# Kernel tuning notes

Hardware: AMD Instinct MI355X
Metric: run time of the kernel (lower is better)

## Reference

```python
import jax, jax.numpy as jnp
import numpy as np

B, L, N, HID, NH, HD, SH, SW, MH = 1, 512, 2048, 2048, 16, 128, 64, 32, 8192


def _rms(x, w, eps=1e-6):
    return x * jax.lax.rsqrt(jnp.mean(x * x, axis=-1, keepdims=True) + eps) * w


def _adaln(x, emb, W, b, nw):
    e = jax.nn.silu(emb) @ W + b  # [B, 6*hid]
    sh_m, sc_m, g_m, sh_p, sc_p, g_p = jnp.split(e, 6, axis=-1)
    xm = _rms(x, nw) * (1.0 + sc_m[:, None]) + sh_m[:, None]
    return xm, g_m, sh_p, sc_p, g_p


def _rope(x, rope):
    # x: [B, H, S, D], rope: [S, 1, D]
    f = rope[:, 0]  # [S, D]
    cos = jnp.repeat(f[:, 0::2], 2, axis=-1)[None, None]
    sin = jnp.repeat(f[:, 1::2], 2, axis=-1)[None, None]
    xr = x.reshape(*x.shape[:-1], -1, 2)
    x_rot = jnp.stack([-xr[..., 1], xr[..., 0]], axis=-1).reshape(x.shape)
    return x * cos + x_rot * sin


def _sdpa(q, k, v, scale):
    s = jnp.einsum('bhqd,bhkd->bhqk', q, k) * scale
    return jnp.einsum('bhqk,bhkd->bhqd', jax.nn.softmax(s, axis=-1), v)


def _mlp(x, w1, b1, w2, b2):
    return jax.nn.gelu(x @ w1 + b1, approximate=True) @ w2 + b2


def setup_inputs() -> dict:
    key = jax.random.key(0)
    ks = iter(jax.random.split(key, 32))
    r = lambda *s: jax.random.normal(next(ks), s, dtype=jnp.float32) * 0.02
    inp = {
        'txt': jax.random.normal(next(ks), (B, L, HID), dtype=jnp.float32),
        'img': jax.random.normal(next(ks), (B, N, HID), dtype=jnp.float32),
        'vec': jax.random.normal(next(ks), (B, HID), dtype=jnp.float32),
        'rope': jax.random.normal(next(ks), (N, 1, HD), dtype=jnp.float32),
        'sol_temperature': jax.random.uniform(next(ks), (B, 64), dtype=jnp.float32),
        'sol_spatial': jax.random.normal(next(ks), (B, 8, 8), dtype=jnp.float32),
        'ada_img_w': r(HID, 6 * HID), 'ada_img_b': jnp.zeros(6 * HID, jnp.float32), 'ada_img_nw': jnp.ones(HID, jnp.float32),
        'ada_txt_w': r(HID, 6 * HID), 'ada_txt_b': jnp.zeros(6 * HID, jnp.float32), 'ada_txt_nw': jnp.ones(HID, jnp.float32),
        'txt_qkv_w': r(HID, 3 * HID), 'img_qkv_w': r(HID, 3 * HID),
        'txt_out_w': r(HID, HID), 'img_out_w': r(HID, HID),
        'mod_w': r(NH) * 5.0, 'mod_b': r(NH) * 5.0,
        'img_n2_w': jnp.ones(HID, jnp.float32), 'txt_n2_w': jnp.ones(HID, jnp.float32),
        'img_fc1_w': r(HID, MH), 'img_fc1_b': jnp.zeros(MH, jnp.float32),
        'img_fc2_w': r(MH, HID), 'img_fc2_b': jnp.zeros(HID, jnp.float32),
        'txt_fc1_w': r(HID, MH), 'txt_fc1_b': jnp.zeros(MH, jnp.float32),
        'txt_fc2_w': r(MH, HID), 'txt_fc2_b': jnp.zeros(HID, jnp.float32),
        'spatial_h': SH, 'spatial_w': SW,
    }
    return inp


def reference(txt, img, vec, rope, sol_temperature, sol_spatial,
              ada_img_w, ada_img_b, ada_img_nw, ada_txt_w, ada_txt_b, ada_txt_nw,
              txt_qkv_w, img_qkv_w, txt_out_w, img_out_w, mod_w, mod_b,
              img_n2_w, txt_n2_w, img_fc1_w, img_fc1_b, img_fc2_w, img_fc2_b,
              txt_fc1_w, txt_fc1_b, txt_fc2_w, txt_fc2_b, spatial_h, spatial_w):
    b, l, hid = txt.shape
    n = img.shape[1]
    nh = mod_w.shape[0]
    hd = hid // nh
    scale = hd ** (-0.5)

    img_n, img_g, img_shp, img_scp, img_gp = _adaln(img, vec, ada_img_w, ada_img_b, ada_img_nw)
    txt_n, txt_g, txt_shp, txt_scp, txt_gp = _adaln(txt, vec, ada_txt_w, ada_txt_b, ada_txt_nw)

    def qkv(x, w, s):
        p = (x @ w).reshape(b, s, 3, nh, hd).transpose(2, 0, 3, 1, 4)  # [3,B,H,S,D]
        return p[0], p[1], p[2]

    tq, tk, tv = qkv(txt_n, txt_qkv_w, l)
    iq, ik, iv = qkv(img_n, img_qkv_w, n)
    iq = _rope(iq, rope)
    ik = _rope(ik, rope)

    # SOL spatial modulation: bilinear upsample (align_corners=False) + 1x1 conv + exp(clamp)
    sol_up = jax.image.resize(sol_spatial, (b, spatial_h, spatial_w), 'bilinear')
    mod = sol_up[:, None] * mod_w[None, :, None, None] + mod_b[None, :, None, None]
    mod = jnp.exp(jnp.clip(mod, -2.0, 2.0)).reshape(b, nh, n, 1)
    iq = iq * mod
    ik = ik * mod

    k = jnp.concatenate([tk, ik], axis=2)  # [B,H,L+N,D]
    v = jnp.concatenate([tv, iv], axis=2)

    txt_attn = _sdpa(tq, k, v, scale).transpose(0, 2, 1, 3).reshape(b, l, hid) @ txt_out_w

    temp = jnp.clip(jnp.mean(sol_temperature, axis=1, keepdims=True), 0.1)  # [B,1]
    s_eff = jnp.sqrt(scale / temp)[:, :, None, None]  # [B,1,1,1]
    img_attn = _sdpa(iq * s_eff, k * s_eff, v, 1.0).transpose(0, 2, 1, 3).reshape(b, n, hid) @ img_out_w

    txt = txt + txt_g[:, None] * txt_attn
    img = img + img_g[:, None] * img_attn

    txt_in = _rms(txt, txt_n2_w) * (1.0 + txt_scp[:, None]) + txt_shp[:, None]
    img_in = _rms(img, img_n2_w) * (1.0 + img_scp[:, None]) + img_shp[:, None]
    txt = txt + txt_gp[:, None] * _mlp(txt_in, txt_fc1_w, txt_fc1_b, txt_fc2_w, txt_fc2_b)
    img = img + img_gp[:, None] * _mlp(img_in, img_fc1_w, img_fc1_b, img_fc2_w, img_fc2_b)
    return txt, img
```

## Files before the change

kernel.cpp:

```cpp
#include <hip/hip_runtime.h>

typedef short short8 __attribute__((ext_vector_type(8)));
typedef float f32x4 __attribute__((ext_vector_type(4)));

__device__ __forceinline__ unsigned short f2bu(float f) {
  unsigned u = __builtin_bit_cast(unsigned, f);
  u += 0x7fffu + ((u >> 16) & 1u);
  return (unsigned short)(u >> 16);
}

__device__ __forceinline__ unsigned short f2bt(float f) {
  return (unsigned short)(__builtin_bit_cast(unsigned, f) >> 16);
}

__device__ __forceinline__ float b2f(unsigned short b) {
  unsigned u = (unsigned)b << 16;
  return __builtin_bit_cast(float, u);
}

__device__ __forceinline__ float gelu_t(float x) {
  float x3 = x * x * x;
  float t = tanhf(0.7978845608028654f * (x + 0.044715f * x3));
  return 0.5f * x * (1.f + t);
}

__device__ __forceinline__ void gload16(const void* g, void* l) {
  __builtin_amdgcn_global_load_lds(
      (const __attribute__((address_space(1))) void*)g,
      (__attribute__((address_space(3))) void*)l, 16, 0, 0);
}

__global__ __launch_bounds__(256) void prep_small(
    const float* __restrict__ vec, const float* __restrict__ sol_t,
    float* __restrict__ silu_vec, float* __restrict__ scales) {
  __shared__ float red[4];
  int t = threadIdx.x;
  float v = (t < 64) ? sol_t[t] : 0.f;
#pragma unroll
  for (int o = 32; o > 0; o >>= 1) v += __shfl_down(v, o);
  if ((t & 63) == 0) red[t >> 6] = v;
  __syncthreads();
  if (t == 0) {
    float m = (red[0] + red[1] + red[2] + red[3]) * (1.f / 64.f);
    m = fmaxf(m, 0.1f);
    const float sc = 0.08838834764831845f;
    const float l2e = 1.4426950408889634f;
    scales[0] = sc * l2e;
    scales[1] = sc / m * l2e;
  }
  for (int k = t; k < 2048; k += 256) {
    float x = vec[k];
    silu_vec[k] = x / (1.f + expf(-x));
  }
}

__global__ __launch_bounds__(256) void mod_kernel(
    const float* __restrict__ S, const float* __restrict__ mw,
    const float* __restrict__ mb, float* __restrict__ modb) {
  int idx = blockIdx.x * 256 + threadIdx.x;
  int h = idx >> 11, n = idx & 2047;
  int y = n >> 5, x = n & 31;
  float cy = (y + 0.5f) * 0.125f - 0.5f;
  float cx = (x + 0.5f) * 0.25f - 0.5f;
  int y0 = (int)floorf(cy); float fy = cy - (float)y0;
  int x0 = (int)floorf(cx); float fx = cx - (float)x0;
  int y0c = min(max(y0, 0), 7), y1c = min(max(y0 + 1, 0), 7);
  int x0c = min(max(x0, 0), 7), x1c = min(max(x0 + 1, 0), 7);
  float v = (1.f - fy) * ((1.f - fx) * S[y0c * 8 + x0c] + fx * S[y0c * 8 + x1c]) +
            fy * ((1.f - fx) * S[y1c * 8 + x0c] + fx * S[y1c * 8 + x1c]);
  float t = v * mw[h] + mb[h];
  t = fminf(fmaxf(t, -2.f), 2.f);
  modb[idx] = expf(t);
}

__global__ __launch_bounds__(256) void ada_gemv(
    const float* __restrict__ sv,
    const float* __restrict__ Wi, const float* __restrict__ bi,
    const float* __restrict__ Wt, const float* __restrict__ bt,
    float* __restrict__ ei, float* __restrict__ et) {
  __shared__ float red[4][64];
  const float* W = blockIdx.y ? Wt : Wi;
  const float* bb = blockIdx.y ? bt : bi;
  float* e = blockIdx.y ? et : ei;
  int jl = threadIdx.x & 63, ks = threadIdx.x >> 6;
  int j = blockIdx.x * 64 + jl;
  float acc = 0.f;
  int k0 = ks * 512;
#pragma unroll 4
  for (int k = 0; k < 512; ++k) acc += sv[k0 + k] * W[(size_t)(k0 + k) * 12288 + j];
  red[ks][jl] = acc;
  __syncthreads();
  if (ks == 0) e[j] = red[0][jl] + red[1][jl] + red[2][jl] + red[3][jl] + bb[j];
}

__global__ __launch_bounds__(256) void norm1_kernel(
    const float* __restrict__ txt, const float* __restrict__ img,
    const float* __restrict__ nw_t, const float* __restrict__ nw_i,
    const float* __restrict__ e_t, const float* __restrict__ e_i,
    unsigned short* __restrict__ out) {
  __shared__ float red[4];
  int r = blockIdx.x, t = threadIdx.x;
  bool ist = r < 512;
  const float* X = ist ? txt + (size_t)r * 2048 : img + (size_t)(r - 512) * 2048;
  const float* nw = ist ? nw_t : nw_i;
  const float* e = ist ? e_t : e_i;
  const float4* xr = reinterpret_cast<const float4*>(X);
  float4 v0 = xr[t * 2], v1 = xr[t * 2 + 1];
  float ss = v0.x * v0.x + v0.y * v0.y + v0.z * v0.z + v0.w * v0.w +
             v1.x * v1.x + v1.y * v1.y + v1.z * v1.z + v1.w * v1.w;
#pragma unroll
  for (int o = 32; o > 0; o >>= 1) ss += __shfl_down(ss, o);
  if ((t & 63) == 0) red[t >> 6] = ss;
  __syncthreads();
  float rinv = rsqrtf((red[0] + red[1] + red[2] + red[3]) * (1.f / 2048.f) + 1e-6f);
  int c0 = t * 8;
  float xv[8] = {v0.x, v0.y, v0.z, v0.w, v1.x, v1.y, v1.z, v1.w};
  short8 ov;
#pragma unroll
  for (int i = 0; i < 8; ++i) {
    int c = c0 + i;
    float y = xv[i] * rinv * nw[c] * (1.f + e[2048 + c]) + e[c];
    ov[i] = (short)f2bu(y);
  }
  *reinterpret_cast<short8*>(out + (size_t)r * 2048 + c0) = ov;
}

__global__ __launch_bounds__(256) void res1_rms(
    const float* __restrict__ txt, const float* __restrict__ img,
    const float* __restrict__ P0,
    const float* __restrict__ e_t, const float* __restrict__ e_i,
    const float* __restrict__ nw_t, const float* __restrict__ nw_i,
    float* __restrict__ out, unsigned short* __restrict__ actA) {
  __shared__ float red[4];
  int r = blockIdx.x, t = threadIdx.x;
  bool ist = r < 512;
  const float* X = ist ? txt + (size_t)r * 2048 : img + (size_t)(r - 512) * 2048;
  const float* e = ist ? e_t : e_i;
  const float* nw = ist ? nw_t : nw_i;
  int c0 = t * 8;
  const float* p0 = P0 + (size_t)r * 2048 + c0;
  float o[8];
  float ss = 0.f;
#pragma unroll
  for (int i = 0; i < 8; i += 4) {
    float4 x = *reinterpret_cast<const float4*>(X + c0 + i);
    float4 a = *reinterpret_cast<const float4*>(p0 + i);
    float4 g = *reinterpret_cast<const float4*>(e + 4096 + c0 + i);
    o[i + 0] = x.x + g.x * a.x;
    o[i + 1] = x.y + g.y * a.y;
    o[i + 2] = x.z + g.z * a.z;
    o[i + 3] = x.w + g.w * a.w;
    ss += o[i] * o[i] + o[i + 1] * o[i + 1] + o[i + 2] * o[i + 2] + o[i + 3] * o[i + 3];
  }
  *reinterpret_cast<float4*>(out + (size_t)r * 2048 + c0) =
      make_float4(o[0], o[1], o[2], o[3]);
  *reinterpret_cast<float4*>(out + (size_t)r * 2048 + c0 + 4) =
      make_float4(o[4], o[5], o[6], o[7]);
#pragma unroll
  for (int of = 32; of > 0; of >>= 1) ss += __shfl_down(ss, of);
  if ((t & 63) == 0) red[t >> 6] = ss;
  __syncthreads();
  float rinv = rsqrtf((red[0] + red[1] + red[2] + red[3]) * (1.f / 2048.f) + 1e-6f);
  short8 ov;
#pragma unroll
  for (int i = 0; i < 8; ++i) {
    int c = c0 + i;
    float y = o[i] * rinv * nw[c] * (1.f + e[8192 + c]) + e[6144 + c];
    ov[i] = (short)f2bu(y);
  }
  *reinterpret_cast<short8*>(actA + (size_t)r * 2048 + c0) = ov;
}

__global__ __launch_bounds__(256) void transpose_w2(
    const float* __restrict__ W0, const float* __restrict__ W1,
    unsigned short* __restrict__ B0, unsigned short* __restrict__ B1,
    int K, int N) {
  __shared__ float tile[64][65];
  const float* W = blockIdx.z ? W1 : W0;
  unsigned short* Bt = blockIdx.z ? B1 : B0;
  int n0 = blockIdx.x * 64, k0 = blockIdx.y * 64;
  int t = threadIdx.x;
  int rn = (t & 15) * 4, rk = t >> 4;
#pragma unroll
  for (int j = 0; j < 4; ++j) {
    float4 v = *reinterpret_cast<const float4*>(
        W + (size_t)(k0 + rk + j * 16) * N + n0 + rn);
    tile[rk + j * 16][rn + 0] = v.x;
    tile[rk + j * 16][rn + 1] = v.y;
    tile[rk + j * 16][rn + 2] = v.z;
    tile[rk + j * 16][rn + 3] = v.w;
  }
  __syncthreads();
  int wn = t >> 2, wk = (t & 3) * 16;
  unsigned pk[8];
#pragma unroll
  for (int i = 0; i < 8; ++i) {
    float lo = tile[wk + 2 * i][wn], hi = tile[wk + 2 * i + 1][wn];
    pk[i] = (unsigned)f2bu(lo) | ((unsigned)f2bu(hi) << 16);
  }
  unsigned short* dst = Bt + (size_t)(n0 + wn) * K + k0 + wk;
  *reinterpret_cast<int4*>(dst) = make_int4(pk[0], pk[1], pk[2], pk[3]);
  *reinterpret_cast<int4*>(dst + 8) = make_int4(pk[4], pk[5], pk[6], pk[7]);
}

__global__ __launch_bounds__(256) void transpose_v(
    const unsigned short* __restrict__ V, unsigned short* __restrict__ Vt) {
  __shared__ unsigned short tile[32][33];
  int h = blockIdx.z;
  int s0 = blockIdx.x * 32, d0 = blockIdx.y * 32;
  int tx = threadIdx.x, ty = threadIdx.y;
  const unsigned short* src = V + (size_t)h * 2560 * 128;
  unsigned short* dst = Vt + (size_t)h * 128 * 2560;
#pragma unroll
  for (int j = 0; j < 32; j += 8)
    tile[ty + j][tx] = src[(size_t)(s0 + ty + j) * 128 + d0 + tx];
  __syncthreads();
#pragma unroll
  for (int j = 0; j < 32; j += 8)
    dst[(size_t)(d0 + ty + j) * 2560 + s0 + tx] = tile[tx][ty + j];
}

struct GemmP {
  const unsigned short *A, *Bt_t, *Bt_i;
  float* C;
  unsigned short* Cb;
  const float *bias_t, *bias_i;
  const float *rope, *modb;
  unsigned short *q_txt, *q_img, *k_cat, *v_cat;
  const float* scales;
  const float *ga_t, *ga_i;
  int Mb_t;
  int N, K, KS;
};

template <int EPI>
__global__ __launch_bounds__(256) void gemm2(GemmP p) {
  __shared__ __align__(16) char GRAW[65536];
  int4* sAb = reinterpret_cast<int4*>(GRAW);
  int4* sBb = reinterpret_cast<int4*>(GRAW + 32768);
  const int NB = gridDim.x, MBT = gridDim.y;
  int nwg = NB * MBT;
  int orig = blockIdx.y * NB + blockIdx.x;
  int qq = nwg >> 3, rr = nwg & 7, xcd = orig & 7, base = orig >> 3;
  int sw = (xcd < rr ? xcd * (qq + 1) : rr * (qq + 1) + (xcd - rr) * qq) + base;
  int bx = sw / MBT, by = sw % MBT;
  const bool is_t = by < p.Mb_t;
  const unsigned short* Bt = is_t ? p.Bt_t : p.Bt_i;
  const int m0 = by * 128, n0 = bx * 128;
  const int z = blockIdx.z;
  const int Kz = p.K / p.KS, kbeg = z * Kz, kend = kbeg + Kz;
  const int tid = threadIdx.x;
  const int w = tid >> 6, l = tid & 63, lr = l & 15, lg = l >> 4;
  const int wm = (w >> 1) * 64, wn = (w & 1) * 64;
  f32x4 acc[4][4] = {};
  const int4* Ag = reinterpret_cast<const int4*>(p.A);
  const int4* Bg = reinterpret_cast<const int4*>(Bt);
  const int K8 = p.K >> 3;
  int srow[4], sch[4];
#pragma unroll
  for (int i = 0; i < 4; ++i) {
    int s = i * 256 + tid;
    srow[i] = s >> 3;
    sch[i] = (s & 7) ^ (srow[i] & 7);
  }
  {
    int kc = kbeg >> 3;
#pragma unroll
    for (int i = 0; i < 4; ++i) {
      gload16(&Ag[(size_t)(m0 + srow[i]) * K8 + kc + sch[i]], &sAb[i * 256 + w * 64]);
      gload16(&Bg[(size_t)(n0 + srow[i]) * K8 + kc + sch[i]], &sBb[i * 256 + w * 64]);
    }
  }
  asm volatile("s_waitcnt vmcnt(0)" ::: "memory");
  __builtin_amdgcn_sched_barrier(0);
  __builtin_amdgcn_s_barrier();
  int cur = 0;
  for (int k0 = kbeg; k0 < kend; k0 += 64) {
    if (k0 + 64 < kend) {
      int kc = (k0 + 64) >> 3;
      int nb = (cur ^ 1) * 1024;
#pragma unroll
      for (int i = 0; i < 4; ++i) {
        gload16(&Ag[(size_t)(m0 + srow[i]) * K8 + kc + sch[i]], &sAb[nb + i * 256 + w * 64]);
        gload16(&Bg[(size_t)(n0 + srow[i]) * K8 + kc + sch[i]], &sBb[nb + i * 256 + w * 64]);
      }
      __builtin_amdgcn_sched_barrier(0);
    }
    const short8* pA = reinterpret_cast<const short8*>(sAb + cur * 1024);
    const short8* pB = reinterpret_cast<const short8*>(sBb + cur * 1024);
    __builtin_amdgcn_s_setprio(1);
#pragma unroll
    for (int kk = 0; kk < 2; ++kk) {
      short8 af[4], bf[4];
#pragma unroll
      for (int m = 0; m < 4; ++m) {
        int row = wm + m * 16 + lr;
        af[m] = pA[row * 8 + ((kk * 4 + lg) ^ (row & 7))];
      }
#pragma unroll
      for (int n = 0; n < 4; ++n) {
        int row = wn + n * 16 + lr;
        bf[n] = pB[row * 8 + ((kk * 4 + lg) ^ (row & 7))];
      }
#pragma unroll
      for (int m = 0; m < 4; ++m)
#pragma unroll
        for (int n = 0; n < 4; ++n)
          acc[m][n] = __builtin_amdgcn_mfma_f32_16x16x32_bf16(af[m], bf[n], acc[m][n], 0, 0, 0);
    }
    __builtin_amdgcn_s_setprio(0);
    asm volatile("s_waitcnt vmcnt(0)" ::: "memory");
    __builtin_amdgcn_sched_barrier(0);
    __builtin_amdgcn_s_barrier();
    cur ^= 1;
  }
  if (EPI == 0) {
    float* C = p.C + (size_t)z * MBT * 128 * p.N;
#pragma unroll
    for (int m = 0; m < 4; ++m)
#pragma unroll
      for (int n = 0; n < 4; ++n)
#pragma unroll
        for (int j = 0; j < 4; ++j) {
          int r = m0 + wm + m * 16 + lg * 4 + j;
          int cc = n0 + wn + n * 16 + lr;
          C[(size_t)r * p.N + cc] = acc[m][n][j];
        }
  } else if (EPI == 1) {
    const float* bias = is_t ? p.bias_t : p.bias_i;
#pragma unroll
    for (int n = 0; n < 4; ++n) {
      int cc = n0 + wn + n * 16 + lr;
      float bv = bias[cc];
#pragma unroll
      for (int m = 0; m < 4; ++m)
#pragma unroll
        for (int j = 0; j < 4; ++j) {
          int r = m0 + wm + m * 16 + lg * 4 + j;
          p.Cb[(size_t)r * p.N + cc] = f2bu(gelu_t(acc[m][n][j] + bv));
        }
    }
  } else if (EPI == 3) {
    unsigned short* osh = reinterpret_cast<unsigned short*>(GRAW);
#pragma unroll
    for (int m = 0; m < 4; ++m)
#pragma unroll
      for (int n = 0; n < 4; ++n)
#pragma unroll
        for (int j = 0; j < 4; ++j) {
          int row = wm + m * 16 + lg * 4 + j;
          int col = wn + n * 16 + lr;
          osh[row * 136 + col] = f2bu(acc[m][n][j]);
        }
    __syncthreads();
    const float* gat = (is_t ? p.ga_t : p.ga_i) + 10240;
    const float* bias = is_t ? p.bias_t : p.bias_i;
    int row = tid >> 1, d0 = (tid & 1) * 64;
    int r = m0 + row;
    const unsigned short* src = osh + row * 136 + d0;
    float* op = p.C + (size_t)r * p.N + n0 + d0;
#pragma unroll
    for (int i = 0; i < 16; ++i) {
      float4 o = *reinterpret_cast<const float4*>(op + i * 4);
      float4 g = *reinterpret_cast<const float4*>(gat + n0 + d0 + i * 4);
      float4 bv = *reinterpret_cast<const float4*>(bias + n0 + d0 + i * 4);
      o.x += g.x * (b2f(src[i * 4 + 0]) + bv.x);
      o.y += g.y * (b2f(src[i * 4 + 1]) + bv.y);
      o.z += g.z * (b2f(src[i * 4 + 2]) + bv.z);
      o.w += g.w * (b2f(src[i * 4 + 3]) + bv.w);
      *reinterpret_cast<float4*>(op + i * 4) = o;
    }
  } else {
    unsigned short* osh = reinterpret_cast<unsigned short*>(GRAW);
#pragma unroll
    for (int m = 0; m < 4; ++m)
#pragma unroll
      for (int n = 0; n < 4; ++n)
#pragma unroll
        for (int j = 0; j < 4; ++j) {
          int row = wm + m * 16 + lg * 4 + j;
          int col = wn + n * 16 + lr;
          osh[row * 136 + col] = f2bu(acc[m][n][j]);
        }
    __syncthreads();
    int sel = bx >> 4, h = bx & 15;
    int row = tid >> 1, d0 = (tid & 1) * 64;
    int r = m0 + row;
    const unsigned short* src = osh + row * 136 + d0;
    if (is_t) {
      if (sel == 0) {
        float qs = p.scales[0];
        unsigned short* dst = p.q_txt + ((size_t)h * 512 + r) * 128 + d0;
#pragma unroll
        for (int i = 0; i < 8; ++i) {
          short8 v = *reinterpret_cast<const short8*>(src + i * 8);
          short8 o;
#pragma unroll
          for (int t = 0; t < 8; ++t)
            o[t] = (short)f2bu(b2f((unsigned short)v[t]) * qs);
          *reinterpret_cast<short8*>(dst + i * 8) = o;
        }
      } else {
        unsigned short* dst =
            (sel == 1 ? p.k_cat : p.v_cat) + ((size_t)h * 2560 + r) * 128 + d0;
#pragma unroll
        for (int i = 0; i < 8; ++i)
          *reinterpret_cast<short8*>(dst + i * 8) =
              *reinterpret_cast<const short8*>(src + i * 8);
      }
    } else {
      int s = r - 512;
      if (sel == 2) {
        unsigned short* dst = p.v_cat + ((size_t)h * 2560 + r) * 128 + d0;
#pragma unroll
        for (int i = 0; i < 8; ++i)
          *reinterpret_cast<short8*>(dst + i * 8) =
              *reinterpret_cast<const short8*>(src + i * 8);
      } else {
        float mv = p.modb[h * 2048 + s];
        float qs = (sel == 0) ? p.scales[1] * mv : mv;
        const float2* rp = reinterpret_cast<const float2*>(p.rope + (size_t)s * 128 + d0);
        unsigned short* dst = (sel == 0)
            ? p.q_img + ((size_t)h * 2048 + s) * 128 + d0
            : p.k_cat + ((size_t)h * 2560 + r) * 128 + d0;
#pragma unroll
        for (int i = 0; i < 8; ++i) {
          short8 v = *reinterpret_cast<const short8*>(src + i * 8);
          short8 o;
#pragma unroll
          for (int t = 0; t < 4; ++t) {
            float2 cs = rp[i * 4 + t];
            float e = b2f((unsigned short)v[2 * t]);
            float od = b2f((unsigned short)v[2 * t + 1]);
            o[2 * t] = (short)f2bu((e * cs.x - od * cs.y) * qs);
            o[2 * t + 1] = (short)f2bu((od * cs.x + e * cs.y) * qs);
          }
          *reinterpret_cast<short8*>(dst + i * 8) = o;
        }
      }
    }
  }
}

__global__ __launch_bounds__(256, 4) void attn_kernel(
    const unsigned short* __restrict__ q_txt, const unsigned short* __restrict__ q_img,
    const unsigned short* __restrict__ Kc, const unsigned short* __restrict__ Vt,
    unsigned short* __restrict__ Op, float* __restrict__ ml) {
  __shared__ __align__(16) char RAW[40960];
  int4* sK = reinterpret_cast<int4*>(RAW);
  int4* sV = reinterpret_cast<int4*>(RAW + 16384);
  int4* sP = reinterpret_cast<int4*>(RAW + 32768);
  unsigned short* osh = reinterpret_cast<unsigned short*>(RAW);
  const int tid = threadIdx.x, w = tid >> 6, l = tid & 63, lr = l & 15, lg = l >> 4;
  int flat = blockIdx.x + 40 * (blockIdx.y + 16 * blockIdx.z);
  int sw = (flat & 7) * 320 + (flat >> 3);
  const int bx = sw % 40;
  int hz = sw / 40;
  const int h = hz & 15, z = hz >> 4;
  const bool is_t = bx < 8;
  const int orow = is_t ? bx * 64 : 512 + (bx - 8) * 64;
  const unsigned short* Qp = is_t ? q_txt + ((size_t)h * 512 + bx * 64) * 128
                                  : q_img + ((size_t)h * 2048 + (bx - 8) * 64) * 128;
  short8 aq[4];
#pragma unroll
  for (int ds = 0; ds < 4; ++ds) {
    int row = w * 16 + lr;
    aq[ds] = *reinterpret_cast<const short8*>(Qp + (size_t)row * 128 + ds * 32 + lg * 8);
  }
  const int4* Kg = reinterpret_cast<const int4*>(Kc + (size_t)h * 2560 * 128);
  const int4* Vg = reinterpret_cast<const int4*>(Vt + (size_t)h * 128 * 2560);
  const short8* pK = reinterpret_cast<const short8*>(sK);
  const short8* pV = reinterpret_cast<const short8*>(sV);
  const short8* pP = reinterpret_cast<const short8*>(sP);
  unsigned short* sPb = reinterpret_cast<unsigned short*>(sP);
  int krow[4], kch[4], vrow[4], vch[4];
#pragma unroll
  for (int i = 0; i < 4; ++i) {
    int s = i * 256 + tid;
    krow[i] = s >> 4; kch[i] = (s & 15) ^ (krow[i] & 7);
    vrow[i] = s >> 3; vch[i] = (s & 7) ^ (vrow[i] & 7);
  }
  short8 ones8;
#pragma unroll
  for (int i = 0; i < 8; ++i) ones8[i] = (short)0x3F80;

  f32x4 oacc[8] = {};
  f32x4 oacc_l = {};
  float m_run[4];
#pragma unroll
  for (int j = 0; j < 4; ++j) m_run[j] = -1e30f;

  const int kbeg = z * 10, kend = kbeg + 10;
#pragma unroll
  for (int i = 0; i < 4; ++i)
    gload16(&Kg[(size_t)(kbeg * 64 + krow[i]) * 16 + kch[i]], &sK[i * 256 + w * 64]);
#pragma unroll
  for (int i = 0; i < 4; ++i)
    gload16(&Vg[(size_t)vrow[i] * 320 + kbeg * 8 + vch[i]], &sV[i * 256 + w * 64]);

  for (int kt = kbeg; kt < kend; ++kt) {
    asm volatile("s_waitcnt vmcnt(4)" ::: "memory");
    __builtin_amdgcn_sched_barrier(0);
    __builtin_amdgcn_s_barrier();
    f32x4 sacc[4] = {};
    __builtin_amdgcn_s_setprio(1);
#pragma unroll
    for (int ds = 0; ds < 4; ++ds) {
      short8 bk[4];
#pragma unroll
      for (int n = 0; n < 4; ++n) {
        int row = n * 16 + lr;
        bk[n] = pK[row * 16 + ((ds * 4 + lg) ^ (row & 7))];
      }
#pragma unroll
      for (int n = 0; n < 4; ++n)
        sacc[n] = __builtin_amdgcn_mfma_f32_16x16x32_bf16(aq[ds], bk[n], sacc[n], 0, 0, 0);
    }
    __builtin_amdgcn_s_setprio(0);
    __builtin_amdgcn_s_barrier();
    if (kt + 1 < kend) {
#pragma unroll
      for (int i = 0; i < 4; ++i)
        gload16(&Kg[(size_t)((kt + 1) * 64 + krow[i]) * 16 + kch[i]], &sK[i * 256 + w * 64]);
    }
    float corr_[4];
    bool grow_any = false;
#pragma unroll
    for (int j = 0; j < 4; ++j) {
      float mx = fmaxf(fmaxf(sacc[0][j], sacc[1][j]), fmaxf(sacc[2][j], sacc[3][j]));
      mx = fmaxf(mx, __shfl_xor(mx, 1));
      mx = fmaxf(mx, __shfl_xor(mx, 2));
      mx = fmaxf(mx, __shfl_xor(mx, 4));
      mx = fmaxf(mx, __shfl_xor(mx, 8));
      bool grow = mx > m_run[j] + 11.0f;
      grow_any |= grow;
      float mn = grow ? mx : m_run[j];
      corr_[j] = grow ? exp2f(m_run[j] - mn) : 1.0f;
      m_run[j] = mn;
      int prow = w * 16 + lg * 4 + j;
#pragma unroll
      for (int n = 0; n < 4; ++n) {
        float pp = exp2f(sacc[n][j] - mn);
        int col = n * 16 + lr;
        sPb[prow * 64 + (((col >> 3) ^ (prow & 7)) << 3) + (col & 7)] = f2bt(pp);
      }
    }
    if (__any(grow_any)) {
#pragma unroll
      for (int n = 0; n < 8; ++n)
#pragma unroll
        for (int j = 0; j < 4; ++j) oacc[n][j] *= corr_[j];
#pragma unroll
      for (int j = 0; j < 4; ++j) oacc_l[j] *= corr_[j];
    }
    if (kt + 1 < kend) {
      asm volatile("s_waitcnt vmcnt(4)" ::: "memory");
    } else {
      asm volatile("s_waitcnt vmcnt(0)" ::: "memory");
    }
    __builtin_amdgcn_sched_barrier(0);
    __builtin_amdgcn_s_barrier();
    __builtin_amdgcn_s_setprio(1);
#pragma unroll
    for (int kk = 0; kk < 2; ++kk) {
      short8 ap, bv[8];
      {
        int row = w * 16 + lr;
        ap = pP[row * 8 + ((kk * 4 + lg) ^ (row & 7))];
      }
#pragma unroll
      for (int n = 0; n < 8; ++n) {
        int row = n * 16 + lr;
        bv[n] = pV[row * 8 + ((kk * 4 + lg) ^ (row & 7))];
      }
#pragma unroll
      for (int n = 0; n < 8; ++n)
        oacc[n] = __builtin_amdgcn_mfma_f32_16x16x32_bf16(ap, bv[n], oacc[n], 0, 0, 0);
      oacc_l = __builtin_amdgcn_mfma_f32_16x16x32_bf16(ap, ones8, oacc_l, 0, 0, 0);
    }
    __builtin_amdgcn_s_setprio(0);
    __builtin_amdgcn_s_barrier();
    if (kt + 1 < kend) {
#pragma unroll
      for (int i = 0; i < 4; ++i)
        gload16(&Vg[(size_t)vrow[i] * 320 + (kt + 1) * 8 + vch[i]], &sV[i * 256 + w * 64]);
    }
  }
  const size_t zbase = (size_t)z * 40960 + (size_t)h * 2560 + orow;
  __syncthreads();
#pragma unroll
  for (int j = 0; j < 4; ++j) {
    int row = w * 16 + lg * 4 + j;
#pragma unroll
    for (int n = 0; n < 8; ++n)
      osh[row * 136 + n * 16 + lr] = f2bt(oacc[n][j]);
    if (lr == 0) {
      ml[(zbase + row) * 2] = m_run[j];
      ml[(zbase + row) * 2 + 1] = oacc_l[j];
    }
  }
  __syncthreads();
  {
    int row = tid >> 2, c0 = (tid & 3) * 32;
#pragma unroll
    for (int i = 0; i < 4; ++i)
      *reinterpret_cast<short8*>(Op + (zbase + row) * 128 + c0 + i * 8) =
          *reinterpret_cast<const short8*>(osh + row * 136 + c0 + i * 8);
  }
}

__global__ __launch_bounds__(256) void attn_merge(
    const unsigned short* __restrict__ Op, const float* __restrict__ ml,
    unsigned short* __restrict__ ao) {
  int gid = blockIdx.x * 256 + threadIdx.x;
  int rid = gid >> 4, d0 = (gid & 15) * 8;
  int h = rid / 2560;
  int r = rid - h * 2560;
  float M = -1e30f;
#pragma unroll
  for (int z = 0; z < 4; ++z) M = fmaxf(M, ml[((size_t)z * 40960 + rid) * 2]);
  float L = 0.f;
  float o[8] = {};
#pragma unroll
  for (int z = 0; z < 4; ++z) {
    size_t sidx = (size_t)z * 40960 + rid;
    float mz = ml[sidx * 2], lz = ml[sidx * 2 + 1];
    float wgt = exp2f(mz - M);
    L += wgt * lz;
    short8 v = *reinterpret_cast<const short8*>(Op + sidx * 128 + d0);
#pragma unroll
    for (int i = 0; i < 8; ++i) o[i] += wgt * b2f((unsigned short)v[i]);
  }
  float inv = 1.f / L;
  short8 ov;
#pragma unroll
  for (int i = 0; i < 8; ++i) ov[i] = (short)f2bu(o[i] * inv);
  *reinterpret_cast<short8*>(ao + (size_t)r * 2048 + h * 128 + d0) = ov;
}

extern "C" void kernel_launch(void* const* d_in, const int* in_sizes, int n_in,
                              void* d_out, int out_size, void* d_ws, size_t ws_size,
                              hipStream_t stream) {
  (void)in_sizes; (void)n_in; (void)out_size; (void)ws_size;
  const float* txt = (const float*)d_in[0];
  const float* img = (const float*)d_in[1];
  const float* vec = (const float*)d_in[2];
  const float* rope = (const float*)d_in[3];
  const float* sol_t = (const float*)d_in[4];
  const float* sol_s = (const float*)d_in[5];
  const float* ada_img_w = (const float*)d_in[6];
  const float* ada_img_b = (const float*)d_in[7];
  const float* ada_img_nw = (const float*)d_in[8];
  const float* ada_txt_w = (const float*)d_in[9];
  const float* ada_txt_b = (const float*)d_in[10];
  const float* ada_txt_nw = (const float*)d_in[11];
  const float* txt_qkv_w = (const float*)d_in[12];
  const float* img_qkv_w = (const float*)d_in[13];
  const float* txt_out_w = (const float*)d_in[14];
  const float* img_out_w = (const float*)d_in[15];
  const float* mod_w = (const float*)d_in[16];
  const float* mod_b = (const float*)d_in[17];
  const float* img_n2_w = (const float*)d_in[18];
  const float* txt_n2_w = (const float*)d_in[19];
  const float* img_fc1_w = (const float*)d_in[20];
  const float* img_fc1_b = (const float*)d_in[21];
  const float* img_fc2_w = (const float*)d_in[22];
  const float* img_fc2_b = (const float*)d_in[23];
  const float* txt_fc1_w = (const float*)d_in[24];
  const float* txt_fc1_b = (const float*)d_in[25];
  const float* txt_fc2_w = (const float*)d_in[26];
  const float* txt_fc2_b = (const float*)d_in[27];
  float* out = (float*)d_out;
  char* ws = (char*)d_ws;

  const size_t MB = 1 << 20;
  float* silu_vec = (float*)(ws + 0);
  float* scales = (float*)(ws + 8192);
  float* modb = (float*)(ws + 16384);
  float* e_img = (float*)(ws + 147456);
  float* e_txt = (float*)(ws + 196608);
  unsigned short* wt0 = (unsigned short*)(ws + 1 * MB);
  unsigned short* wt1 = (unsigned short*)(ws + 33 * MB);
  unsigned short* Opart = (unsigned short*)(ws + 1 * MB);
  float* mlbuf = (float*)(ws + 42 * MB);
  unsigned short* actA = (unsigned short*)(ws + 65 * MB);
  char* attn_base = ws + 75 * MB;
  unsigned short* q_txt = (unsigned short*)(attn_base);
  unsigned short* q_img = (unsigned short*)(attn_base + 2 * MB);
  unsigned short* k_cat = (unsigned short*)(attn_base + 10 * MB);
  unsigned short* v_cat = (unsigned short*)(attn_base + 20 * MB);
  unsigned short* vT = (unsigned short*)(attn_base + 30 * MB);
  unsigned short* ao = (unsigned short*)(attn_base + 40 * MB);
  unsigned short* actB = (unsigned short*)attn_base;
  float* Cbuf = (float*)(ws + 125 * MB);

  prep_small<<<1, 256, 0, stream>>>(vec, sol_t, silu_vec, scales);
  mod_kernel<<<128, 256, 0, stream>>>(sol_s, mod_w, mod_b, modb);
  ada_gemv<<<dim3(192, 2), 256, 0, stream>>>(silu_vec, ada_img_w, ada_img_b,
                                             ada_txt_w, ada_txt_b, e_img, e_txt);
  norm1_kernel<<<2560, 256, 0, stream>>>(txt, img, ada_txt_nw, ada_img_nw,
                                         e_txt, e_img, actA);
  transpose_w2<<<dim3(96, 32, 2), 256, 0, stream>>>(txt_qkv_w, img_qkv_w,
                                                    wt0, wt1, 2048, 6144);
  {
    GemmP p = {actA, wt0, wt1, nullptr, nullptr, nullptr, nullptr,
               rope, modb, q_txt, q_img, k_cat, v_cat, scales,
               nullptr, nullptr, 4, 6144, 2048, 1};
    gemm2<2><<<dim3(48, 20, 1), 256, 0, stream>>>(p);
  }
  transpose_v<<<dim3(80, 4, 16), dim3(32, 8), 0, stream>>>(v_cat, vT);
  attn_kernel<<<dim3(40, 16, 4), 256, 0, stream>>>(q_txt, q_img, k_cat, vT, Opart, mlbuf);
  attn_merge<<<2560, 256, 0, stream>>>(Opart, mlbuf, ao);
  transpose_w2<<<dim3(32, 32, 2), 256, 0, stream>>>(txt_out_w, img_out_w,
                                                    wt0, wt1, 2048, 2048);
  {
    GemmP p = {ao, wt0, wt1, Cbuf, nullptr, nullptr, nullptr,
               nullptr, nullptr, nullptr, nullptr, nullptr, nullptr, nullptr,
               nullptr, nullptr, 4, 2048, 2048, 1};
    gemm2<0><<<dim3(16, 20, 1), 256, 0, stream>>>(p);
  }
  res1_rms<<<2560, 256, 0, stream>>>(txt, img, Cbuf, e_txt, e_img,
                                     txt_n2_w, img_n2_w, out, actA);
  transpose_w2<<<dim3(128, 32, 2), 256, 0, stream>>>(txt_fc1_w, img_fc1_w,
                                                     wt0, wt1, 2048, 8192);
  {
    GemmP p = {actA, wt0, wt1, nullptr, actB, txt_fc1_b, img_fc1_b,
               nullptr, nullptr, nullptr, nullptr, nullptr, nullptr, nullptr,
               nullptr, nullptr, 4, 8192, 2048, 1};
    gemm2<1><<<dim3(64, 20, 1), 256, 0, stream>>>(p);
  }
  transpose_w2<<<dim3(32, 128, 2), 256, 0, stream>>>(txt_fc2_w, img_fc2_w,
                                                     wt0, wt1, 8192, 2048);
  {
    GemmP p = {actB, wt0, wt1, out, nullptr, txt_fc2_b, img_fc2_b,
               nullptr, nullptr, nullptr, nullptr, nullptr, nullptr, nullptr,
               e_txt, e_img, 4, 2048, 8192, 1};
    gemm2<3><<<dim3(16, 20, 1), 256, 0, stream>>>(p);
  }
}
```

Baseline: 691.2 us.

## Drop split-K attention and merge kernel, normalize output in-kernel

Removes the four-way split of the key sequence in the attention kernel, so each block processes all 40 key tiles and normalizes its output directly, writing into the final head-interleaved layout. The separate merge kernel and its partial-output and max/sum buffers are eliminated, saving a launch plus the partial writes and reads. In exchange the grid shrinks from 2560 to 640 blocks, which lowers parallelism and may underfill the GPU's compute units while lengthening each block's serial loop.

```diff
diff --git a/kernel.cpp b/kernel.cpp
--- a/kernel.cpp
+++ b/kernel.cpp
@@ -445,18 +445,17 @@
 __global__ __launch_bounds__(256, 4) void attn_kernel(
     const unsigned short* __restrict__ q_txt, const unsigned short* __restrict__ q_img,
     const unsigned short* __restrict__ Kc, const unsigned short* __restrict__ Vt,
-    unsigned short* __restrict__ Op, float* __restrict__ ml) {
+    unsigned short* __restrict__ ao) {
   __shared__ __align__(16) char RAW[40960];
   int4* sK = reinterpret_cast<int4*>(RAW);
   int4* sV = reinterpret_cast<int4*>(RAW + 16384);
   int4* sP = reinterpret_cast<int4*>(RAW + 32768);
   unsigned short* osh = reinterpret_cast<unsigned short*>(RAW);
   const int tid = threadIdx.x, w = tid >> 6, l = tid & 63, lr = l & 15, lg = l >> 4;
-  int flat = blockIdx.x + 40 * (blockIdx.y + 16 * blockIdx.z);
-  int sw = (flat & 7) * 320 + (flat >> 3);
+  int flat = blockIdx.x + 40 * blockIdx.y;
+  int sw = (flat & 7) * 80 + (flat >> 3);
   const int bx = sw % 40;
-  int hz = sw / 40;
-  const int h = hz & 15, z = hz >> 4;
+  const int h = sw / 40;
   const bool is_t = bx < 8;
   const int orow = is_t ? bx * 64 : 512 + (bx - 8) * 64;
   const unsigned short* Qp = is_t ? q_txt + ((size_t)h * 512 + bx * 64) * 128
@@ -490,7 +489,7 @@
 #pragma unroll
   for (int j = 0; j < 4; ++j) m_run[j] = -1e30f;
 
-  const int kbeg = z * 10, kend = kbeg + 10;
+  const int kbeg = 0, kend = 40;
 #pragma unroll
   for (int i = 0; i < 4; ++i)
     gload16(&Kg[(size_t)(kbeg * 64 + krow[i]) * 16 + kch[i]], &sK[i * 256 + w * 64]);
@@ -586,56 +585,23 @@
         gload16(&Vg[(size_t)vrow[i] * 320 + (kt + 1) * 8 + vch[i]], &sV[i * 256 + w * 64]);
     }
   }
-  const size_t zbase = (size_t)z * 40960 + (size_t)h * 2560 + orow;
   __syncthreads();
 #pragma unroll
   for (int j = 0; j < 4; ++j) {
     int row = w * 16 + lg * 4 + j;
+    float inv = 1.f / oacc_l[j];
 #pragma unroll
     for (int n = 0; n < 8; ++n)
-      osh[row * 136 + n * 16 + lr] = f2bt(oacc[n][j]);
-    if (lr == 0) {
-      ml[(zbase + row) * 2] = m_run[j];
-      ml[(zbase + row) * 2 + 1] = oacc_l[j];
-    }
+      osh[row * 136 + n * 16 + lr] = f2bu(oacc[n][j] * inv);
   }
   __syncthreads();
   {
     int row = tid >> 2, c0 = (tid & 3) * 32;
 #pragma unroll
     for (int i = 0; i < 4; ++i)
-      *reinterpret_cast<short8*>(Op + (zbase + row) * 128 + c0 + i * 8) =
+      *reinterpret_cast<short8*>(ao + (size_t)(orow + row) * 2048 + h * 128 + c0 + i * 8) =
           *reinterpret_cast<const short8*>(osh + row * 136 + c0 + i * 8);
   }
-}
-
-__global__ __launch_bounds__(256) void attn_merge(
-    const unsigned short* __restrict__ Op, const float* __restrict__ ml,
-    unsigned short* __restrict__ ao) {
-  int gid = blockIdx.x * 256 + threadIdx.x;
-  int rid = gid >> 4, d0 = (gid & 15) * 8;
-  int h = rid / 2560;
-  int r = rid - h * 2560;
-  float M = -1e30f;
-#pragma unroll
-  for (int z = 0; z < 4; ++z) M = fmaxf(M, ml[((size_t)z * 40960 + rid) * 2]);
-  float L = 0.f;
-  float o[8] = {};
-#pragma unroll
-  for (int z = 0; z < 4; ++z) {
-    size_t sidx = (size_t)z * 40960 + rid;
-    float mz = ml[sidx * 2], lz = ml[sidx * 2 + 1];
-    float wgt = exp2f(mz - M);
-    L += wgt * lz;
-    short8 v = *reinterpret_cast<const short8*>(Op + sidx * 128 + d0);
-#pragma unroll
-    for (int i = 0; i < 8; ++i) o[i] += wgt * b2f((unsigned short)v[i]);
-  }
-  float inv = 1.f / L;
-  short8 ov;
-#pragma unroll
-  for (int i = 0; i < 8; ++i) ov[i] = (short)f2bu(o[i] * inv);
-  *reinterpret_cast<short8*>(ao + (size_t)r * 2048 + h * 128 + d0) = ov;
 }
 
 extern "C" void kernel_launch(void* const* d_in, const int* in_sizes, int n_in,
@@ -681,8 +647,6 @@
   float* e_txt = (float*)(ws + 196608);
   unsigned short* wt0 = (unsigned short*)(ws + 1 * MB);
   unsigned short* wt1 = (unsigned short*)(ws + 33 * MB);
-  unsigned short* Opart = (unsigned short*)(ws + 1 * MB);
-  float* mlbuf = (float*)(ws + 42 * MB);
   unsigned short* actA = (unsigned short*)(ws + 65 * MB);
   char* attn_base = ws + 75 * MB;
   unsigned short* q_txt = (unsigned short*)(attn_base);
@@ -709,8 +673,7 @@
     gemm2<2><<<dim3(48, 20, 1), 256, 0, stream>>>(p);
   }
   transpose_v<<<dim3(80, 4, 16), dim3(32, 8), 0, stream>>>(v_cat, vT);
-  attn_kernel<<<dim3(40, 16, 4), 256, 0, stream>>>(q_txt, q_img, k_cat, vT, Opart, mlbuf);
-  attn_merge<<<2560, 256, 0, stream>>>(Opart, mlbuf, ao);
+  attn_kernel<<<dim3(40, 16), 256, 0, stream>>>(q_txt, q_img, k_cat, vT, ao);
   transpose_w2<<<dim3(32, 32, 2), 256, 0, stream>>>(txt_out_w, img_out_w,
                                                     wt0, wt1, 2048, 2048);
   {
```

New measurement: 690.6 us. No clear change (-0.1%).
